# Kernel tuning notes

Hardware: AMD Instinct MI355X
Metric: run time of the kernel (lower is better)

The kernel has to match this reference:

```python
import jax, jax.numpy as jnp
import numpy as np

D = 1024
H = 16
DH = D // H
B, T = 2, 2048


def setup_inputs() -> dict:
    key = jax.random.key(0)
    ks = jax.random.split(key, 5)
    x = jax.random.normal(ks[0], (B, T, D), dtype=jnp.float32)
    # torch nn.Linear init scale ~ 1/sqrt(fan_in)
    sc = 1.0 / np.sqrt(D)
    W_qkv = jax.random.uniform(ks[1], (3 * D, D), dtype=jnp.float32, minval=-sc, maxval=sc)
    b_qkv = jax.random.uniform(ks[2], (3 * D,), dtype=jnp.float32, minval=-sc, maxval=sc)
    W_o = jax.random.uniform(ks[3], (D, D), dtype=jnp.float32, minval=-sc, maxval=sc)
    b_o = jax.random.uniform(ks[4], (D,), dtype=jnp.float32, minval=-sc, maxval=sc)
    return {"x": x, "W_qkv": W_qkv, "b_qkv": b_qkv, "W_o": W_o, "b_o": b_o}


def reference(x, W_qkv, b_qkv, W_o, b_o):
    Bx, Tx, C = x.shape
    scale = DH ** -0.5
    qkv = x @ W_qkv.T + b_qkv                       # [B,T,3D]
    qkv = qkv.reshape(Bx, Tx, 3, H, DH)
    q, k, v = jnp.moveaxis(qkv, 2, 0)               # each [B,T,H,DH]
    q = q.transpose(0, 2, 1, 3)                     # [B,H,T,DH]
    k = k.transpose(0, 2, 1, 3)
    v = v.transpose(0, 2, 1, 3)
    scores = jnp.einsum("bhqd,bhkd->bhqk", q, k) * scale
    a = jax.nn.softmax(scores, axis=-1)
    o = jnp.einsum("bhqk,bhkd->bhqd", a, v)         # [B,H,T,DH]
    o = o.transpose(0, 2, 1, 3).reshape(Bx, Tx, C)
    return o @ W_o.T + b_o
```

## Files before the change

kernel.cpp:

```cpp
#include <hip/hip_runtime.h>

#define TT 2048
#define DD 1024
#define HH 16
#define DHH 64

typedef __attribute__((ext_vector_type(4)))  float  f32x4;
typedef __attribute__((ext_vector_type(16))) float  f32x16;
typedef __attribute__((ext_vector_type(8)))  short  bf16x8;
typedef __attribute__((ext_vector_type(4)))  float  f4;
typedef __attribute__((ext_vector_type(4)))  unsigned short u16x4;
typedef __attribute__((ext_vector_type(4)))  unsigned int   u32x4;

__device__ __forceinline__ unsigned short f2b(float f) {
    union { float f; unsigned int u; } v; v.f = f;
    unsigned int r = v.u + 0x7fffu + ((v.u >> 16) & 1u);
    return (unsigned short)(r >> 16);
}

__device__ __forceinline__ void gl_lds16(const void* g, void* l) {
    __builtin_amdgcn_global_load_lds(
        (const __attribute__((address_space(1))) unsigned int*)g,
        (__attribute__((address_space(3))) unsigned int*)l, 16, 0, 0);
}

__device__ __forceinline__ f32x16 mfma32(bf16x8 a, bf16x8 b, f32x16 c) {
    return __builtin_amdgcn_mfma_f32_32x32x16_bf16(a, b, c, 0, 0, 0);
}

__device__ __forceinline__ float fexp2(float x) {
    float r; asm("v_exp_f32 %0, %1" : "=v"(r) : "v"(x)); return r;
}

__device__ __forceinline__ unsigned int pkbf(float a, float b) {
    unsigned int r;
    asm("v_cvt_pk_bf16_f32 %0, %1, %2" : "=v"(r) : "v"(a), "v"(b));
    return r;
}

__device__ __forceinline__ void pl32swap(unsigned int& a, unsigned int& b) {
    asm("v_permlane32_swap_b32 %0, %1" : "+v"(a), "+v"(b));
}

__device__ __forceinline__ bf16x8 u2h(u32x4 u) {
    union { u32x4 u; bf16x8 h; } x; x.u = u; return x.h;
}

__global__ void f2b3_kernel(const float* __restrict__ x, const float* __restrict__ wq,
                            const float* __restrict__ wo, unsigned short* __restrict__ d) {
    int i = blockIdx.x * blockDim.x + threadIdx.x;
    const float* s; int off;
    if (i < 1048576)      { s = x;  off = i; }
    else if (i < 1835008) { s = wq; off = i - 1048576; }
    else                  { s = wo; off = i - 1835008; }
    f4 v = ((const f4*)s)[off];
    u16x4 o;
    o[0] = f2b(v[0]); o[1] = f2b(v[1]); o[2] = f2b(v[2]); o[3] = f2b(v[3]);
    ((u16x4*)d)[i] = o;
}

template<int BN, int MODE>
__global__ __launch_bounds__(256) void gemm_bt(
    const unsigned short* __restrict__ A, const unsigned short* __restrict__ Bm,
    const float* __restrict__ bias, int N, int K,
    unsigned short* __restrict__ q, unsigned short* __restrict__ k,
    unsigned short* __restrict__ vt, float* __restrict__ outf)
{
    constexpr int NB  = BN / 32;
    constexpr int ASZ = 128 * 32;
    constexpr int BSZ = BN * 32;
    constexpr int BNCH = (MODE == 0 ? 12 : 8);
    __shared__ unsigned short lds[2 * (ASZ + BSZ)];

    int tid = threadIdx.x;
    int l = tid & 63, w = tid >> 6;
    int wr = w >> 1, wc = w & 1;
    int lr = l & 15, lk = (l >> 4) * 8;

    int lin = blockIdx.x;
    int cx = lin & 7, ii = lin >> 3;
    int bm = (cx >> 1) * 8 + (ii & 7);
    int bn = (cx & 1) * BNCH + (ii >> 3);

    f32x4 acc[4][NB] = {};

    const unsigned short* Ag = A + (size_t)(bm * 128) * K;
    const unsigned short* Bg = Bm + (size_t)(bn * BN) * K;

    auto stage = [&](int buf, int k0) {
        unsigned short* As = lds + buf * (ASZ + BSZ);
        unsigned short* Bs = As + ASZ;
#pragma unroll
        for (int r = 0; r < 2; ++r) {
            int e = r * 256 + tid;
            int row = e >> 2, kc = (e & 3) * 8;
            gl_lds16(Ag + (size_t)row * K + k0 + kc, &As[e * 8]);
        }
#pragma unroll
        for (int r = 0; r < BN / 64; ++r) {
            int e = r * 256 + tid;
            int row = e >> 2, kc = (e & 3) * 8;
            gl_lds16(Bg + (size_t)row * K + k0 + kc, &Bs[e * 8]);
        }
    };

    stage(0, 0);
    __syncthreads();
    int cur = 0;
    for (int k0 = 0; k0 < K; k0 += 32) {
        if (k0 + 32 < K) stage(cur ^ 1, k0 + 32);
        const unsigned short* As = lds + cur * (ASZ + BSZ);
        const unsigned short* Bs = As + ASZ;
        bf16x8 a[4], b[NB];
#pragma unroll
        for (int i = 0; i < 4; ++i)
            a[i] = *(const bf16x8*)&As[(wr * 64 + i * 16 + lr) * 32 + lk];
#pragma unroll
        for (int j = 0; j < NB; ++j)
            b[j] = *(const bf16x8*)&Bs[(wc * (BN / 2) + j * 16 + lr) * 32 + lk];
        __builtin_amdgcn_s_setprio(1);
#pragma unroll
        for (int i = 0; i < 4; ++i)
#pragma unroll
            for (int j = 0; j < NB; ++j)
                acc[i][j] = __builtin_amdgcn_mfma_f32_16x16x32_bf16(a[i], b[j], acc[i][j], 0, 0, 0);
        __builtin_amdgcn_s_setprio(0);
        __syncthreads();
        cur ^= 1;
    }

#pragma unroll
    for (int i = 0; i < 4; ++i) {
#pragma unroll
        for (int j = 0; j < NB; ++j) {
            int row0 = bm * 128 + wr * 64 + i * 16 + (l >> 4) * 4;
            int col  = bn * BN + wc * (BN / 2) + j * 16 + (l & 15);
            float bv = bias[col];
            float val[4];
#pragma unroll
            for (int r = 0; r < 4; ++r) val[r] = acc[i][j][r] + bv;
            if (MODE == 0) {
                int which = col >> 10, rem = col & 1023;
                int h = rem >> 6, d = rem & 63;
                int b = row0 >> 11, t0 = row0 & 2047;
                if (which == 0) {
#pragma unroll
                    for (int r = 0; r < 4; ++r)
                        q[((size_t)((b * HH + h) * TT + t0 + r)) * DHH + d] =
                            f2b(val[r] * 0.18033688011112042f);
                } else if (which == 1) {
#pragma unroll
                    for (int r = 0; r < 4; ++r)
                        k[((size_t)((b * HH + h) * TT + t0 + r)) * DHH + d] = f2b(val[r]);
                } else {
                    u16x4 pk;
#pragma unroll
                    for (int r = 0; r < 4; ++r) pk[r] = f2b(val[r]);
                    *(u16x4*)(vt + ((size_t)((b * HH + h) * DHH + d)) * TT + t0) = pk;
                }
            } else {
#pragma unroll
                for (int r = 0; r < 4; ++r)
                    outf[(size_t)(row0 + r) * N + col] = val[r];
            }
        }
    }
}

__global__ __launch_bounds__(512, 4) void attn(
    const unsigned short* __restrict__ qb,
    const unsigned short* __restrict__ kb,
    const unsigned short* __restrict__ vtb,
    unsigned short* __restrict__ ob)
{
    extern __shared__ char lds[];

    int tid = threadIdx.x;
    int l = tid & 63, w = tid >> 6;
    int g = w >> 2, wg = w & 3;
    int hi = l >> 5, c = l & 31;
    int tig = tid & 255;

    int lin = blockIdx.x;
    int swz = (lin & 7) * 64 + (lin >> 3);
    int bh = swz >> 4;
    int qrow = (swz & 15) * 128 + wg * 32 + c;

    bf16x8 qf[4];
    const unsigned short* qg = qb + ((size_t)bh * TT + qrow) * DHH;
#pragma unroll
    for (int kd = 0; kd < 4; ++kd)
        qf[kd] = *(const bf16x8*)(qg + kd * 16 + hi * 8);

    f32x16 oa0 = {}, oa1 = {};
    float m = -1e30f, lsum = 0.f;

    const char* kgl = (const char*)(kb + (size_t)bh * TT * DHH) + (size_t)g * 1024 * 128;
    const char* vgl = (const char*)(vtb + (size_t)bh * DHH * TT) + (size_t)g * 1024 * 2;
    char* base = lds + g * 16384;

    for (int kt0 = 0; kt0 < 1024; kt0 += 64) {
#pragma unroll
        for (int r = 0; r < 2; ++r) {
            int p = r * 4096 + tig * 16;
            int rw = p >> 7, qq = p & 127;
            int sw = qq ^ ((rw & 7) << 4);
            gl_lds16(kgl + (size_t)(kt0 + rw) * 128 + sw, base + p);
            gl_lds16(vgl + (size_t)rw * (TT * 2) + kt0 * 2 + sw, base + 8192 + p);
        }
        __syncthreads();
        const char* Ksb = base;
        const char* Vsb = base + 8192;

        f32x16 s0 = {}, s1 = {};
        __builtin_amdgcn_s_setprio(1);
#pragma unroll
        for (int kd = 0; kd < 4; ++kd) {
            int cb = (kd * 16 + hi * 8) * 2;
            int xr = cb ^ ((c & 7) << 4);
            bf16x8 kf0 = *(const bf16x8*)(Ksb + c * 128 + xr);
            bf16x8 kf1 = *(const bf16x8*)(Ksb + (32 + c) * 128 + xr);
            s0 = mfma32(kf0, qf[kd], s0);
            s1 = mfma32(kf1, qf[kd], s1);
        }
        __builtin_amdgcn_s_setprio(0);

        float mx0 = fmaxf(fmaxf(s0[0], s0[1]), s0[2]);
        float mx1 = fmaxf(fmaxf(s0[3], s0[4]), s0[5]);
        float mx2 = fmaxf(fmaxf(s0[6], s0[7]), s0[8]);
        float mx3 = fmaxf(fmaxf(s0[9], s0[10]), s0[11]);
        float mx4 = fmaxf(fmaxf(s0[12], s0[13]), s0[14]);
        float mx5 = fmaxf(fmaxf(s0[15], s1[0]), s1[1]);
        float mx6 = fmaxf(fmaxf(s1[2], s1[3]), s1[4]);
        float mx7 = fmaxf(fmaxf(s1[5], s1[6]), s1[7]);
        float mx8 = fmaxf(fmaxf(s1[8], s1[9]), s1[10]);
        float mx9 = fmaxf(fmaxf(s1[11], s1[12]), s1[13]);
        float mxA = fmaxf(s1[14], s1[15]);
        float t0 = fmaxf(fmaxf(mx0, mx1), mx2);
        float t1 = fmaxf(fmaxf(mx3, mx4), mx5);
        float t2 = fmaxf(fmaxf(mx6, mx7), mx8);
        float t3 = fmaxf(mx9, mxA);
        float tm = fmaxf(fmaxf(t0, t1), fmaxf(t2, t3));
        tm = fmaxf(tm, __shfl_xor(tm, 32, 64));

        float nm = fmaxf(m, tm);
        if (!__all(nm - m <= 8.f)) {
            float corr = fexp2(m - nm);
            lsum *= corr;
#pragma unroll
            for (int r = 0; r < 16; ++r) { oa0[r] *= corr; oa1[r] *= corr; }
            m = nm;
        }

        float p4[4] = {0.f, 0.f, 0.f, 0.f};
#pragma unroll
        for (int r = 0; r < 16; ++r) { s0[r] = fexp2(s0[r] - m); p4[r & 3] += s0[r]; }
#pragma unroll
        for (int r = 0; r < 16; ++r) { s1[r] = fexp2(s1[r] - m); p4[r & 3] += s1[r]; }
        lsum += (p4[0] + p4[1]) + (p4[2] + p4[3]);

        u32x4 pf0, pf1, pf2, pf3;
#define MKFRAG(sv, base_, dst) { \
        unsigned int c0 = pkbf(sv[base_+0], sv[base_+1]); \
        unsigned int c1 = pkbf(sv[base_+2], sv[base_+3]); \
        unsigned int c2 = pkbf(sv[base_+4], sv[base_+5]); \
        unsigned int c3 = pkbf(sv[base_+6], sv[base_+7]); \
        pl32swap(c0, c2); pl32swap(c1, c3); \
        dst[0] = c0; dst[1] = c1; dst[2] = c2; dst[3] = c3; }
        MKFRAG(s0, 0, pf0)
        MKFRAG(s0, 8, pf1)
        MKFRAG(s1, 0, pf2)
        MKFRAG(s1, 8, pf3)
#undef MKFRAG

        __builtin_amdgcn_s_setprio(1);
#define PVSTEP(kc, pf) { \
        int cb = (kc * 16 + hi * 8) * 2; \
        int xr = ((c & 7) << 4); \
        bf16x8 vf0 = *(const bf16x8*)(Vsb + c * 128 + (cb ^ xr)); \
        bf16x8 vf1 = *(const bf16x8*)(Vsb + (32 + c) * 128 + (cb ^ xr)); \
        bf16x8 ph = u2h(pf); \
        oa0 = mfma32(vf0, ph, oa0); \
        oa1 = mfma32(vf1, ph, oa1); }
        PVSTEP(0, pf0)
        PVSTEP(1, pf1)
        PVSTEP(2, pf2)
        PVSTEP(3, pf3)
#undef PVSTEP
        __builtin_amdgcn_s_setprio(0);

        __syncthreads();
    }

    float* Om = (float*)lds;
    float* ml = (float*)(lds + 32768);
    if (g == 1) {
        float* o = Om + wg * 2048 + l;
#pragma unroll
        for (int r = 0; r < 16; ++r) o[r * 64]        = oa0[r];
#pragma unroll
        for (int r = 0; r < 16; ++r) o[(16 + r) * 64] = oa1[r];
        ml[wg * 128 + l]      = m;
        ml[wg * 128 + 64 + l] = lsum;
    }
    __syncthreads();
    if (g == 1) return;

    float m2 = ml[wg * 128 + l];
    float l2 = ml[wg * 128 + 64 + l];
    float M  = fmaxf(m, m2);
    float a1 = fexp2(m - M), a2 = fexp2(m2 - M);
    float Lh = lsum * a1 + l2 * a2;
    float L  = Lh + __shfl_xor(Lh, 32, 64);
    float rn = 1.0f / L;
    const float* o2 = Om + wg * 2048 + l;

    int b = bh >> 4, h = bh & 15;
    unsigned short* obase = ob + ((size_t)(b * TT + qrow)) * DD + h * 64;
#pragma unroll
    for (int gq = 0; gq < 4; ++gq) {
        u16x4 o0, o1;
#pragma unroll
        for (int e = 0; e < 4; ++e) {
            int r = gq * 4 + e;
            o0[e] = f2b((oa0[r] * a1 + o2[r * 64] * a2) * rn);
            o1[e] = f2b((oa1[r] * a1 + o2[(16 + r) * 64] * a2) * rn);
        }
        *(u16x4*)(obase + 8 * gq + 4 * hi)      = o0;
        *(u16x4*)(obase + 32 + 8 * gq + 4 * hi) = o1;
    }
}

extern "C" void kernel_launch(void* const* d_in, const int* in_sizes, int n_in,
                              void* d_out, int out_size, void* d_ws, size_t ws_size,
                              hipStream_t stream) {
    const float* x    = (const float*)d_in[0];
    const float* Wqkv = (const float*)d_in[1];
    const float* bqkv = (const float*)d_in[2];
    const float* Wo   = (const float*)d_in[3];
    const float* bo   = (const float*)d_in[4];
    float* out = (float*)d_out;

    unsigned short* xb  = (unsigned short*)d_ws;
    unsigned short* wqb = xb  + 4096 * 1024;
    unsigned short* wob = wqb + 3072 * 1024;
    unsigned short* q   = wob + 1024 * 1024;
    unsigned short* k   = q   + 2 * 16 * 2048 * 64;
    unsigned short* vt  = k   + 2 * 16 * 2048 * 64;
    unsigned short* ob  = vt  + 2 * 16 * 2048 * 64;

    f2b3_kernel<<<dim3(8192), dim3(256), 0, stream>>>(x, Wqkv, Wo, xb);

    gemm_bt<128, 0><<<dim3(768), dim3(256), 0, stream>>>(xb, wqb, bqkv, 3072, 1024,
                                                         q, k, vt, nullptr);
    attn<<<dim3(512), dim3(512), 34816, stream>>>(q, k, vt, ob);

    gemm_bt<64, 1><<<dim3(512), dim3(256), 0, stream>>>(ob, wob, bo, 1024, 1024,
                                                        nullptr, nullptr, nullptr, out);
}
```

Baseline: 111.0 us.

## Double-buffer K/V tiles in attention with async global-to-LDS prefetch

The attention kernel now uses two LDS buffers per split-K group. It prefetches the next K/V tile with global_load_lds while the current tile is consumed, and uses explicit vmcnt waits and raw barriers in place of __syncthreads. The goal is to hide global load latency behind the QK and PV MFMA work. In exchange, LDS per block rises from about 34 KB to 64 KB, which may lower occupancy per CU.

```diff
diff --git a/kernel.cpp b/kernel.cpp
--- a/kernel.cpp
+++ b/kernel.cpp
@@ -44,6 +44,12 @@
 
 __device__ __forceinline__ bf16x8 u2h(u32x4 u) {
     union { u32x4 u; bf16x8 h; } x; x.u = u; return x.h;
+}
+
+__device__ __forceinline__ void bar() {
+    asm volatile("" ::: "memory");
+    __builtin_amdgcn_s_barrier();
+    asm volatile("" ::: "memory");
 }
 
 __global__ void f2b3_kernel(const float* __restrict__ x, const float* __restrict__ wq,
@@ -197,20 +203,34 @@
 
     const char* kgl = (const char*)(kb + (size_t)bh * TT * DHH) + (size_t)g * 1024 * 128;
     const char* vgl = (const char*)(vtb + (size_t)bh * DHH * TT) + (size_t)g * 1024 * 2;
-    char* base = lds + g * 16384;
-
-    for (int kt0 = 0; kt0 < 1024; kt0 += 64) {
+    char* base = lds + g * 32768;
+
+    auto stage = [&](int buf, int kt0) {
+        char* bb = base + buf * 16384;
 #pragma unroll
         for (int r = 0; r < 2; ++r) {
             int p = r * 4096 + tig * 16;
             int rw = p >> 7, qq = p & 127;
             int sw = qq ^ ((rw & 7) << 4);
-            gl_lds16(kgl + (size_t)(kt0 + rw) * 128 + sw, base + p);
-            gl_lds16(vgl + (size_t)rw * (TT * 2) + kt0 * 2 + sw, base + 8192 + p);
-        }
-        __syncthreads();
-        const char* Ksb = base;
-        const char* Vsb = base + 8192;
+            gl_lds16(kgl + (size_t)(kt0 + rw) * 128 + sw, bb + p);
+            gl_lds16(vgl + (size_t)rw * (TT * 2) + kt0 * 2 + sw, bb + 8192 + p);
+        }
+    };
+
+    stage(0, 0);
+    int cur = 0;
+
+    for (int kt0 = 0; kt0 < 1024; kt0 += 64) {
+        if (kt0 + 64 < 1024) {
+            stage(cur ^ 1, kt0 + 64);
+            asm volatile("s_waitcnt vmcnt(4)" ::: "memory");
+        } else {
+            asm volatile("s_waitcnt vmcnt(0)" ::: "memory");
+        }
+        __builtin_amdgcn_s_barrier();
+        asm volatile("" ::: "memory");
+        const char* Ksb = base + cur * 16384;
+        const char* Vsb = Ksb + 8192;
 
         f32x16 s0 = {}, s1 = {};
         __builtin_amdgcn_s_setprio(1);
@@ -289,7 +309,8 @@
 #undef PVSTEP
         __builtin_amdgcn_s_setprio(0);
 
-        __syncthreads();
+        bar();
+        cur ^= 1;
     }
 
     float* Om = (float*)lds;
@@ -353,7 +374,7 @@
 
     gemm_bt<128, 0><<<dim3(768), dim3(256), 0, stream>>>(xb, wqb, bqkv, 3072, 1024,
                                                          q, k, vt, nullptr);
-    attn<<<dim3(512), dim3(512), 34816, stream>>>(q, k, vt, ob);
+    attn<<<dim3(512), dim3(512), 65536, stream>>>(q, k, vt, ob);
 
     gemm_bt<64, 1><<<dim3(512), dim3(256), 0, stream>>>(ob, wob, bo, 1024, 1024,
                                                         nullptr, nullptr, nullptr, out);
```

New measurement: 109.9 us. No clear change (-1.0%).

## Split attention KV range across four wave groups with tree reduction

Applied to the files above, without the earlier changes.

Doubles the attention block to 1024 threads so four wave groups each process a quarter of the key sequence instead of two groups each taking half. Partial softmax states (max, sum, output accumulators) are merged in two LDS reduction stages before group 0 normalizes and writes the output. The goal is more parallelism and latency hiding per head/query tile. In exchange the block needs twice the LDS, adds extra synchronization and merge work, and the stricter launch bounds may force register spills.

```diff
diff --git a/kernel.cpp b/kernel.cpp
--- a/kernel.cpp
+++ b/kernel.cpp
@@ -167,7 +167,7 @@
     }
 }
 
-__global__ __launch_bounds__(512, 4) void attn(
+__global__ __launch_bounds__(1024, 8) void attn(
     const unsigned short* __restrict__ qb,
     const unsigned short* __restrict__ kb,
     const unsigned short* __restrict__ vtb,
@@ -195,11 +195,11 @@
     f32x16 oa0 = {}, oa1 = {};
     float m = -1e30f, lsum = 0.f;
 
-    const char* kgl = (const char*)(kb + (size_t)bh * TT * DHH) + (size_t)g * 1024 * 128;
-    const char* vgl = (const char*)(vtb + (size_t)bh * DHH * TT) + (size_t)g * 1024 * 2;
+    const char* kgl = (const char*)(kb + (size_t)bh * TT * DHH) + (size_t)g * 512 * 128;
+    const char* vgl = (const char*)(vtb + (size_t)bh * DHH * TT) + (size_t)g * 512 * 2;
     char* base = lds + g * 16384;
 
-    for (int kt0 = 0; kt0 < 1024; kt0 += 64) {
+    for (int kt0 = 0; kt0 < 512; kt0 += 64) {
 #pragma unroll
         for (int r = 0; r < 2; ++r) {
             int p = r * 4096 + tig * 16;
@@ -293,8 +293,35 @@
     }
 
     float* Om = (float*)lds;
-    float* ml = (float*)(lds + 32768);
-    if (g == 1) {
+    float* ml = (float*)(lds + 65536);
+
+    if (g & 1) {
+        int slot = g >> 1;
+        float* o = Om + slot * 8192 + wg * 2048 + l;
+#pragma unroll
+        for (int r = 0; r < 16; ++r) o[r * 64]        = oa0[r];
+#pragma unroll
+        for (int r = 0; r < 16; ++r) o[(16 + r) * 64] = oa1[r];
+        ml[slot * 512 + wg * 128 + l]      = m;
+        ml[slot * 512 + wg * 128 + 64 + l] = lsum;
+    }
+    __syncthreads();
+    if (!(g & 1)) {
+        int slot = g >> 1;
+        float m2 = ml[slot * 512 + wg * 128 + l];
+        float l2 = ml[slot * 512 + wg * 128 + 64 + l];
+        float M  = fmaxf(m, m2);
+        float a1 = fexp2(m - M), a2 = fexp2(m2 - M);
+        lsum = lsum * a1 + l2 * a2;
+        const float* o2 = Om + slot * 8192 + wg * 2048 + l;
+#pragma unroll
+        for (int r = 0; r < 16; ++r) oa0[r] = oa0[r] * a1 + o2[r * 64] * a2;
+#pragma unroll
+        for (int r = 0; r < 16; ++r) oa1[r] = oa1[r] * a1 + o2[(16 + r) * 64] * a2;
+        m = M;
+    }
+    __syncthreads();
+    if (g == 2) {
         float* o = Om + wg * 2048 + l;
 #pragma unroll
         for (int r = 0; r < 16; ++r) o[r * 64]        = oa0[r];
@@ -304,30 +331,32 @@
         ml[wg * 128 + 64 + l] = lsum;
     }
     __syncthreads();
-    if (g == 1) return;
-
-    float m2 = ml[wg * 128 + l];
-    float l2 = ml[wg * 128 + 64 + l];
-    float M  = fmaxf(m, m2);
-    float a1 = fexp2(m - M), a2 = fexp2(m2 - M);
-    float Lh = lsum * a1 + l2 * a2;
-    float L  = Lh + __shfl_xor(Lh, 32, 64);
-    float rn = 1.0f / L;
-    const float* o2 = Om + wg * 2048 + l;
-
-    int b = bh >> 4, h = bh & 15;
-    unsigned short* obase = ob + ((size_t)(b * TT + qrow)) * DD + h * 64;
-#pragma unroll
-    for (int gq = 0; gq < 4; ++gq) {
-        u16x4 o0, o1;
-#pragma unroll
-        for (int e = 0; e < 4; ++e) {
-            int r = gq * 4 + e;
-            o0[e] = f2b((oa0[r] * a1 + o2[r * 64] * a2) * rn);
-            o1[e] = f2b((oa1[r] * a1 + o2[(16 + r) * 64] * a2) * rn);
-        }
-        *(u16x4*)(obase + 8 * gq + 4 * hi)      = o0;
-        *(u16x4*)(obase + 32 + 8 * gq + 4 * hi) = o1;
+    if (g != 0) return;
+
+    {
+        float m2 = ml[wg * 128 + l];
+        float l2 = ml[wg * 128 + 64 + l];
+        float M  = fmaxf(m, m2);
+        float a1 = fexp2(m - M), a2 = fexp2(m2 - M);
+        float Lh = lsum * a1 + l2 * a2;
+        float L  = Lh + __shfl_xor(Lh, 32, 64);
+        float rn = 1.0f / L;
+        const float* o2 = Om + wg * 2048 + l;
+
+        int b = bh >> 4, h = bh & 15;
+        unsigned short* obase = ob + ((size_t)(b * TT + qrow)) * DD + h * 64;
+#pragma unroll
+        for (int gq = 0; gq < 4; ++gq) {
+            u16x4 o0, o1;
+#pragma unroll
+            for (int e = 0; e < 4; ++e) {
+                int r = gq * 4 + e;
+                o0[e] = f2b((oa0[r] * a1 + o2[r * 64] * a2) * rn);
+                o1[e] = f2b((oa1[r] * a1 + o2[(16 + r) * 64] * a2) * rn);
+            }
+            *(u16x4*)(obase + 8 * gq + 4 * hi)      = o0;
+            *(u16x4*)(obase + 32 + 8 * gq + 4 * hi) = o1;
+        }
     }
 }
 
@@ -353,7 +382,7 @@
 
     gemm_bt<128, 0><<<dim3(768), dim3(256), 0, stream>>>(xb, wqb, bqkv, 3072, 1024,
                                                          q, k, vt, nullptr);
-    attn<<<dim3(512), dim3(512), 34816, stream>>>(q, k, vt, ob);
+    attn<<<dim3(512), dim3(1024), 69632, stream>>>(q, k, vt, ob);
 
     gemm_bt<64, 1><<<dim3(512), dim3(256), 0, stream>>>(ob, wob, bo, 1024, 1024,
                                                         nullptr, nullptr, nullptr, out);
```

After: 345.0 us. 3.11x slower.
